# Optimization experiments

Hardware: AMD Instinct MI355X
Metric: run time of the kernel (lower is better)

## Reference

```python
import jax, jax.numpy as jnp
import numpy as np

# Cubic B-spline weights at integer offsets: B3(0)=2/3, B3(+-1)=1/6.
# grid_pull(input, identity_grid, interpolation=3, bound='zero') reduces to a
# separable 3-tap filter [1/6, 4/6, 1/6] along each spatial axis with zero padding.
W0 = 2.0 / 3.0
W1 = 1.0 / 6.0


def _cubic_filter_axis(x, axis):
    pad = [(0, 0)] * x.ndim
    pad[axis] = (1, 1)  # bound='zero': out-of-range coefficients are zero
    xp = jnp.pad(x, pad)
    n = x.shape[axis]
    left = jax.lax.slice_in_dim(xp, 0, n, axis=axis)    # c[i-1]
    mid = jax.lax.slice_in_dim(xp, 1, n + 1, axis=axis)  # c[i]
    right = jax.lax.slice_in_dim(xp, 2, n + 2, axis=axis)  # c[i+1]
    return W1 * left + W0 * mid + W1 * right


def setup_inputs() -> dict:
    key = jax.random.key(0)
    coeff = jax.random.normal(key, (2, 2, 160, 192, 160), dtype=jnp.float32)
    return {"coeff": coeff}


def reference(coeff):
    # coeff: (batch, channel, D, H, W) spline coefficients -> values at voxels
    out = coeff
    for ax in range(2, coeff.ndim):
        out = _cubic_filter_axis(out, ax)
    return out
```

## Files before the change

### kernel.cpp

```cpp
#include <hip/hip_runtime.h>


typedef float f32x2 __attribute__((ext_vector_type(2)));

static constexpr int Dd = 160, Hh = 192, Ww = 160, BC = 4;
static constexpr int Zt = 8, Yt = 16;
static constexpr int NZB = Dd / Zt;
static constexpr int NYB = Hh / Yt;
static constexpr float KW1 = 1.0f / 6.0f;
static constexpr float KW0 = 2.0f / 3.0f;

static constexpr int ROWF   = 164;
static constexpr int PATCHF = 18 * ROWF;

__device__ __forceinline__ void gload16(const float* g, float* l) {
    __builtin_amdgcn_global_load_lds(
        (const __attribute__((address_space(1))) float*)g,
        (__attribute__((address_space(3))) float*)l, 16, 0, 0);
}

struct YF { float v[12]; };

__global__ __launch_bounds__(256) void CoeffToValue_kernel(
    const float* __restrict__ in, float* __restrict__ out)
{
    __shared__ __align__(16) float lds[2 * PATCHF + 4];

    const int tid  = threadIdx.x;
    const int lane = tid & 63;
    const int wave = tid >> 6;
    const int wc   = tid & 15;
    const int yo   = tid >> 4;

    const int bid = blockIdx.x;
    const int zc  = bid % NZB;
    const int yb  = (bid / NZB) % NYB;
    const int bc  = bid / (NZB * NYB);
    const int z0  = zc * Zt;
    const int y0  = yb * Yt;

    float cyw[3];
    {
        const float wy[3] = {KW1, KW0, KW1};
#pragma unroll
        for (int dy = 0; dy < 3; ++dy) {
            const int g = y0 + yo + dy - 1;
            cyw[dy] = (g >= 0 && g < Hh) ? wy[dy] : 0.0f;
        }
    }

    const size_t plane = (size_t)Hh * Ww;
    const float* inb = in + (size_t)bc * Dd * plane;

    auto stage = [&](int k) {
        int zs = z0 + k;
        zs = zs < 0 ? 0 : (zs >= Dd ? Dd - 1 : zs);
        const float* sp = inb + (size_t)zs * plane;
        float* slot = lds + (k & 1) * PATCHF;
        if (lane < 40) {
            for (int p = wave; p < 18; p += 4) {
                int ys = y0 - 1 + p;
                ys = ys < 0 ? 0 : (ys >= Hh ? Hh - 1 : ys);
                gload16(sp + (size_t)ys * Ww + lane * 4, slot + p * ROWF + 4);
            }
        }
    };

    auto yfilter = [&](int k) -> YF {
        const float* base = lds + (k & 1) * PATCHF + 10 * wc + 2;
        YF o;
#pragma unroll
        for (int q = 0; q < 12; ++q) o.v[q] = 0.0f;
#pragma unroll
        for (int dy = 0; dy < 3; ++dy) {
            const float* rp = base + (yo + dy) * ROWF;
            float v[14];
#pragma unroll
            for (int r = 0; r < 7; ++r) {
                f32x2 p2 = *reinterpret_cast<const f32x2*>(rp + 2 * r);
                v[2 * r] = p2.x; v[2 * r + 1] = p2.y;
            }
            const float c = cyw[dy];
#pragma unroll
            for (int q = 0; q < 12; ++q) o.v[q] = fmaf(c, v[q + 1], o.v[q]);
        }
        return o;
    };

    stage(-1); stage(0);
    __syncthreads();
    YF a = yfilter(-1);
    YF b = yfilter(0);
    __syncthreads();
    stage(1);
    __syncthreads();

#pragma unroll
    for (int i = 0; i < Zt; ++i) {
        if (i < Zt - 1) stage(i + 2);

        YF n = yfilter(i + 1);

        const int z = z0 + i;
        const float czm = (z > 0)      ? KW1 : 0.0f;
        const float czp = (z < Dd - 1) ? KW1 : 0.0f;

        float t[12];
#pragma unroll
        for (int q = 0; q < 12; ++q)
            t[q] = fmaf(czm, a.v[q], fmaf(KW0, b.v[q], czp * n.v[q]));
        t[0]  = (wc > 0)  ? t[0]  : 0.0f;
        t[11] = (wc < 15) ? t[11] : 0.0f;

        float* orow = out + ((size_t)(bc * Dd + z) * Hh + (y0 + yo)) * Ww + 10 * wc;
#pragma unroll
        for (int s = 0; s < 5; ++s) {
            f32x2 o2;
            o2.x = fmaf(KW0, t[2 * s + 1], KW1 * (t[2 * s]     + t[2 * s + 2]));
            o2.y = fmaf(KW0, t[2 * s + 2], KW1 * (t[2 * s + 1] + t[2 * s + 3]));
            *reinterpret_cast<f32x2*>(orow + 2 * s) = o2;
        }

        a = b; b = n;

        if (i < Zt - 1) __syncthreads();
    }
}

extern "C" void kernel_launch(void* const* d_in, const int* in_sizes, int n_in,
                              void* d_out, int out_size, void* d_ws, size_t ws_size,
                              hipStream_t stream) {
    const float* in = (const float*)d_in[0];
    float* out = (float*)d_out;

    const int blocks = BC * NYB * NZB;
    CoeffToValue_kernel<<<blocks, 256, 0, stream>>>(in, out);
}
```

Measured before the change: 34.06 us.

## Triple-buffer LDS z-slices with vmcnt-based waits instead of full syncthreads

```diff
diff --git a/kernel.cpp b/kernel.cpp
--- a/kernel.cpp
+++ b/kernel.cpp
@@ -11,7 +11,11 @@
 static constexpr float KW0 = 2.0f / 3.0f;
 
 static constexpr int ROWF   = 164;
-static constexpr int PATCHF = 18 * ROWF;
+static constexpr int PROWS  = 20;
+static constexpr int PATCHF = PROWS * ROWF;
+
+#define VMCNT(n) asm volatile("s_waitcnt vmcnt(" #n ")" ::: "memory")
+#define BAR()    __builtin_amdgcn_s_barrier()
 
 __device__ __forceinline__ void gload16(const float* g, float* l) {
     __builtin_amdgcn_global_load_lds(
@@ -21,10 +25,10 @@
 
 struct YF { float v[12]; };
 
-__global__ __launch_bounds__(256) void CoeffToValue_kernel(
+__global__ __launch_bounds__(256, 4) void CoeffToValue_kernel(
     const float* __restrict__ in, float* __restrict__ out)
 {
-    __shared__ __align__(16) float lds[2 * PATCHF + 4];
+    __shared__ __align__(16) float lds[3 * PATCHF];
 
     const int tid  = threadIdx.x;
     const int lane = tid & 63;
@@ -52,22 +56,27 @@
     const size_t plane = (size_t)Hh * Ww;
     const float* inb = in + (size_t)bc * Dd * plane;
 
+    const int woff = (lane == 0) ? 0 : 4 * (lane - 1);
+
     auto stage = [&](int k) {
         int zs = z0 + k;
         zs = zs < 0 ? 0 : (zs >= Dd ? Dd - 1 : zs);
         const float* sp = inb + (size_t)zs * plane;
-        float* slot = lds + (k & 1) * PATCHF;
-        if (lane < 40) {
-            for (int p = wave; p < 18; p += 4) {
-                int ys = y0 - 1 + p;
+        float* slot = lds + ((k + 3) % 3) * PATCHF;
+        if (lane < 41) {
+#pragma unroll
+            for (int r = 0; r < 5; ++r) {
+                const int p  = wave + 4 * r;
+                const int ps = p > 17 ? 17 : p;
+                int ys = y0 - 1 + ps;
                 ys = ys < 0 ? 0 : (ys >= Hh ? Hh - 1 : ys);
-                gload16(sp + (size_t)ys * Ww + lane * 4, slot + p * ROWF + 4);
+                gload16(sp + (size_t)ys * Ww + woff, slot + p * ROWF);
             }
         }
     };
 
     auto yfilter = [&](int k) -> YF {
-        const float* base = lds + (k & 1) * PATCHF + 10 * wc + 2;
+        const float* base = lds + ((k + 3) % 3) * PATCHF + 10 * wc + 2;
         YF o;
 #pragma unroll
         for (int q = 0; q < 12; ++q) o.v[q] = 0.0f;
@@ -87,18 +96,18 @@
         return o;
     };
 
-    stage(-1); stage(0);
-    __syncthreads();
+    stage(-1); stage(0); stage(1);
+    VMCNT(10); BAR();
     YF a = yfilter(-1);
+    VMCNT(5); BAR();
+    stage(2);
     YF b = yfilter(0);
-    __syncthreads();
-    stage(1);
-    __syncthreads();
 
 #pragma unroll
     for (int i = 0; i < Zt; ++i) {
-        if (i < Zt - 1) stage(i + 2);
-
+        if (i == 0) { VMCNT(5); } else { VMCNT(10); }
+        BAR();
+        if (i <= Zt - 3) stage(i + 3);
         YF n = yfilter(i + 1);
 
         const int z = z0 + i;
@@ -122,8 +131,6 @@
         }
 
         a = b; b = n;
-
-        if (i < Zt - 1) __syncthreads();
     }
 }
 
```

Result: no change. 33.48 us (-1.7%).
